# Optimization experiments

Measured on AMD Instinct MI355X. Metric: run time of the kernel, lower is better.

The kernel has to match this reference:

```python
import jax, jax.numpy as jnp
import numpy as np

NUM_ITEMS = 100000
D_SEM = 768
D_PROMPT = 384
D_MODEL = 2048
B, T = 64, 200


def setup_inputs() -> dict:
    key = jax.random.key(0)
    k_ids, k_len, k_sem, k_vp, k_w = jax.random.split(key, 5)
    ids = jax.random.randint(k_ids, (B, T), 0, NUM_ITEMS, dtype=jnp.int64 if jax.config.jax_enable_x64 else jnp.int32)
    lengths = jax.random.randint(k_len, (B,), 1, T + 1, dtype=ids.dtype)
    # positions beyond each sequence length are padding (-1), as produced by the dataloader
    pos = jnp.arange(T, dtype=ids.dtype)[None, :]
    ids = jnp.where(pos < lengths[:, None], ids, -1)
    E_sem = jax.random.normal(k_sem, (NUM_ITEMS, D_SEM), dtype=jnp.float32)
    v_prompt = 0.02 * jax.random.normal(k_vp, (NUM_ITEMS, D_PROMPT), dtype=jnp.float32)
    # nn.Linear weight: [out_features, in_features]
    proj_w = jax.random.normal(k_w, (D_MODEL, D_SEM + D_PROMPT), dtype=jnp.float32) * (1.0 / np.sqrt(D_SEM + D_PROMPT))
    return {"batch_item_ids_padded": ids, "batch_lengths": lengths,
            "E_sem": E_sem, "v_prompt": v_prompt, "proj_w": proj_w}


def reference(batch_item_ids_padded, batch_lengths, E_sem, v_prompt, proj_w):
    """Vectorized build_inputs_embeds: gather + concat + projection, masked.
    Returns (embeds [B,T,d_model], amask [B,T], tok_item_ids [B,T])."""
    ids = batch_item_ids_padded
    num_items = E_sem.shape[0]
    valid = (ids >= 0) & (ids < num_items)            # [B,T]
    safe = jnp.where(valid, ids, 0)                   # clamp for safe gather
    sem = E_sem[safe]                                 # [B,T,d_sem]
    vp = v_prompt[safe]                               # [B,T,d_prompt]
    cat = jnp.concatenate([sem, vp], axis=-1)         # [B,T,d_sem+d_prompt]
    tok = jnp.einsum('btk,dk->btd', cat, proj_w)      # [B,T,d_model]
    embeds = jnp.where(valid[..., None], tok, jnp.zeros((), tok.dtype))
    amask = valid.astype(jnp.int32)
    tok_item_ids = jnp.where(valid, ids, -1)
    return embeds, amask, tok_item_ids
```

## Files before the change

kernel.cpp:

```cpp
#include <hip/hip_runtime.h>
#include <stdint.h>

constexpr int BB = 64, TT = 200;
constexpr int M  = BB * TT;
constexpr int DSEM = 768, DPR = 384;
constexpr int Kd = DSEM + DPR;
constexpr int Nd = 2048;
constexpr int NUM_ITEMS = 100000;
constexpr int BK = 64;

constexpr int GATHER_BLOCKS = (M * Kd / 8) / 256;
constexpr int WCONV_BLOCKS  = (Nd * Kd / 8) / 256;
constexpr int MASK_BLOCKS   = (M + 255) / 256;

typedef short bf16x8 __attribute__((ext_vector_type(8)));
typedef float f32x4  __attribute__((ext_vector_type(4)));

__device__ __forceinline__ unsigned short f2bf(float f) {
  union { float f; uint32_t u; } v; v.f = f;
  uint32_t u = v.u;
  u += 0x7fffu + ((u >> 16) & 1u);
  return (unsigned short)(u >> 16);
}

__global__ void prep_kernel(const int* __restrict__ ids,
                            const float* __restrict__ Esem,
                            const float* __restrict__ vpr,
                            const float* __restrict__ pw,
                            unsigned short* __restrict__ A,
                            unsigned short* __restrict__ Wb,
                            float* __restrict__ amask,
                            float* __restrict__ tok) {
  const int b = blockIdx.x;
  const int tid = threadIdx.x;
  if (b < GATHER_BLOCKS) {
    unsigned g = (unsigned)b * 256u + tid;
    unsigned row = g / 144u;
    unsigned col = (g - row * 144u) * 8u;
    int id = ids[row];
    bool valid = (id >= 0) && (id < NUM_ITEMS);
    int safe = valid ? id : 0;
    const float* src = (col < (unsigned)DSEM)
                         ? (Esem + (size_t)safe * DSEM + col)
                         : (vpr  + (size_t)safe * DPR  + (col - DSEM));
    float4 v0 = *(const float4*)src;
    float4 v1 = *(const float4*)(src + 4);
    if (!valid) {
      v0.x = v0.y = v0.z = v0.w = 0.f;
      v1.x = v1.y = v1.z = v1.w = 0.f;
    }
    ushort4 o0, o1;
    o0.x = f2bf(v0.x); o0.y = f2bf(v0.y); o0.z = f2bf(v0.z); o0.w = f2bf(v0.w);
    o1.x = f2bf(v1.x); o1.y = f2bf(v1.y); o1.z = f2bf(v1.z); o1.w = f2bf(v1.w);
    unsigned short* dst = A + (size_t)row * Kd + col;
    *(ushort4*)dst       = o0;
    *(ushort4*)(dst + 4) = o1;
  } else if (b < GATHER_BLOCKS + WCONV_BLOCKS) {
    int g = (b - GATHER_BLOCKS) * 256 + tid;
    int e = g * 8;
    float4 v0 = *(const float4*)(pw + e);
    float4 v1 = *(const float4*)(pw + e + 4);
    ushort4 o0, o1;
    o0.x = f2bf(v0.x); o0.y = f2bf(v0.y); o0.z = f2bf(v0.z); o0.w = f2bf(v0.w);
    o1.x = f2bf(v1.x); o1.y = f2bf(v1.y); o1.z = f2bf(v1.z); o1.w = f2bf(v1.w);
    *(ushort4*)(Wb + e)     = o0;
    *(ushort4*)(Wb + e + 4) = o1;
  } else {
    int i = (b - GATHER_BLOCKS - WCONV_BLOCKS) * 256 + tid;
    if (i < M) {
      int id = ids[i];
      bool valid = (id >= 0) && (id < NUM_ITEMS);
      amask[i] = valid ? 1.0f : 0.0f;
      tok[i]   = valid ? (float)id : -1.0f;
    }
  }
}

__device__ __forceinline__ void async16(const void* gsrc, void* ldst) {
  __builtin_amdgcn_global_load_lds(
      (const __attribute__((address_space(1))) unsigned int*)gsrc,
      (__attribute__((address_space(3))) unsigned int*)ldst,
      16, 0, 0);
}

__global__ __launch_bounds__(256) void gemm_kernel(const unsigned short* __restrict__ A,
                                                   const unsigned short* __restrict__ Wb,
                                                   float* __restrict__ C) {
  __shared__ __align__(16) unsigned short lds_a[128 * BK];
  __shared__ __align__(16) unsigned short lds_b[128 * BK];

  const int tid  = threadIdx.x;
  const int lane = tid & 63;
  const int wave = tid >> 6;
  const int wm = wave >> 1, wn = wave & 1;
  const int quad = lane >> 4, lm = lane & 15;

  const int b  = blockIdx.x;
  const int k8 = b & 7;
  const int i  = b >> 3;
  const int m0 = (i >> 1) * 128;
  const int n0 = (k8 + 8 * (i & 1)) * 128;

  const int srow   = tid >> 3;
  const int schunk = tid & 7;

  f32x4 acc[4][4];
#pragma unroll
  for (int i2 = 0; i2 < 4; ++i2)
#pragma unroll
    for (int j = 0; j < 4; ++j) acc[i2][j] = (f32x4){0.f, 0.f, 0.f, 0.f};

  for (int kt = 0; kt < Kd / BK; ++kt) {
    const int k0 = kt * BK;
#pragma unroll
    for (int r = 0; r < 4; ++r) {
      const int row = r * 32 + srow;
      const int gch = schunk ^ (row & 7);
      const unsigned short* ga = A + (size_t)(m0 + row) * Kd + k0 + gch * 8;
      async16(ga, lds_a + (size_t)(r * 256 + wave * 64) * 8);
      const unsigned short* gb = Wb + (size_t)(n0 + row) * Kd + k0 + gch * 8;
      async16(gb, lds_b + (size_t)(r * 256 + wave * 64) * 8);
    }
    __syncthreads();

#pragma unroll
    for (int h = 0; h < 2; ++h) {
      bf16x8 af[4], bfr[4];
#pragma unroll
      for (int mi = 0; mi < 4; ++mi) {
        const int row = wm * 64 + mi * 16 + lm;
        af[mi] = *(const bf16x8*)(lds_a + row * BK + ((h * 4 + quad) ^ (row & 7)) * 8);
      }
#pragma unroll
      for (int ni = 0; ni < 4; ++ni) {
        const int row = wn * 64 + ni * 16 + lm;
        bfr[ni] = *(const bf16x8*)(lds_b + row * BK + ((h * 4 + quad) ^ (row & 7)) * 8);
      }
#pragma unroll
      for (int mi = 0; mi < 4; ++mi)
#pragma unroll
        for (int ni = 0; ni < 4; ++ni)
          acc[mi][ni] = __builtin_amdgcn_mfma_f32_16x16x32_bf16(af[mi], bfr[ni], acc[mi][ni], 0, 0, 0);
    }
    __syncthreads();
  }

  float* lw = (float*)lds_a + wave * 1024;
  const int r4  = lane >> 4;
  const int c16 = lane & 15;
#pragma unroll
  for (int mi = 0; mi < 4; ++mi) {
#pragma unroll
    for (int ni = 0; ni < 4; ++ni)
#pragma unroll
      for (int ii = 0; ii < 4; ++ii)
        lw[(quad * 4 + ii) * 64 + ni * 16 + lm] = acc[mi][ni][ii];
#pragma unroll
    for (int j = 0; j < 4; ++j) {
      float4 v = *(const float4*)(lw + (j * 4 + r4) * 64 + c16 * 4);
      const int row = m0 + wm * 64 + mi * 16 + j * 4 + r4;
      const int col = n0 + wn * 64 + c16 * 4;
      *(float4*)(C + (size_t)row * Nd + col) = v;
    }
  }
}

extern "C" void kernel_launch(void* const* d_in, const int* in_sizes, int n_in,
                              void* d_out, int out_size, void* d_ws, size_t ws_size,
                              hipStream_t stream) {
  const int*   ids  = (const int*)d_in[0];
  const float* Esem = (const float*)d_in[2];
  const float* vpr  = (const float*)d_in[3];
  const float* pw   = (const float*)d_in[4];

  float* out_emb   = (float*)d_out;
  float* out_amask = out_emb + (size_t)M * Nd;
  float* out_tok   = out_amask + M;

  unsigned short* A  = (unsigned short*)d_ws;
  unsigned short* Wb = A + (size_t)M * Kd;

  prep_kernel<<<GATHER_BLOCKS + WCONV_BLOCKS + MASK_BLOCKS, 256, 0, stream>>>(
      ids, Esem, vpr, pw, A, Wb, out_amask, out_tok);
  gemm_kernel<<<(M / 128) * (Nd / 128), 256, 0, stream>>>(A, Wb, out_emb);
}
```

Baseline: 519.4 us.

## Compact valid rows before gather and GEMM, zero-fill padded rows separately

Adds a single-block compaction kernel that uses a ballot-based prefix sum to build lists of valid and invalid row indices. The gather and GEMM then run only over the compacted valid rows: early-exit blocks skip strips beyond the valid count, and outputs are scattered through the index map. Extra blocks write zeros to the padded rows. This removes gather and matmul work on padding, at the cost of an extra serial single-block kernel launch and scattered output writes.

```diff
diff --git a/kernel.cpp b/kernel.cpp
--- a/kernel.cpp
+++ b/kernel.cpp
@@ -11,9 +11,11 @@
 
 constexpr int GATHER_BLOCKS = (M * Kd / 8) / 256;
 constexpr int WCONV_BLOCKS  = (Nd * Kd / 8) / 256;
-constexpr int MASK_BLOCKS   = (M + 255) / 256;
+constexpr int GEMM_BLOCKS   = (M / 128) * (Nd / 128);
+constexpr int ZB            = 256;
 
 typedef short bf16x8 __attribute__((ext_vector_type(8)));
+typedef unsigned short u16x8 __attribute__((ext_vector_type(8)));
 typedef float f32x4  __attribute__((ext_vector_type(4)));
 
 __device__ __forceinline__ unsigned short f2bf(float f) {
@@ -23,56 +25,94 @@
   return (unsigned short)(u >> 16);
 }
 
-__global__ void prep_kernel(const int* __restrict__ ids,
-                            const float* __restrict__ Esem,
-                            const float* __restrict__ vpr,
-                            const float* __restrict__ pw,
-                            unsigned short* __restrict__ A,
-                            unsigned short* __restrict__ Wb,
-                            float* __restrict__ amask,
-                            float* __restrict__ tok) {
+__global__ __launch_bounds__(1024) void compact_kernel(
+    const int* __restrict__ ids,
+    int* __restrict__ cid,
+    int* __restrict__ orig,
+    int* __restrict__ inv,
+    int* __restrict__ cnt,
+    float* __restrict__ amask,
+    float* __restrict__ tok) {
+  __shared__ int wb_v[16], wb_i[16];
+  __shared__ int base_v, base_i;
+  const int tid  = threadIdx.x;
+  const int wave = tid >> 6;
+  const int lane = tid & 63;
+  if (tid == 0) { base_v = 0; base_i = 0; }
+  __syncthreads();
+  const unsigned long long below = (lane == 0) ? 0ull : (~0ull >> (64 - lane));
+  for (int r0 = 0; r0 < M; r0 += 1024) {
+    const int i = r0 + tid;
+    int id = -1;
+    if (i < M) id = ids[i];
+    const bool valid   = (id >= 0) && (id < NUM_ITEMS);
+    const bool invalidRow = (i < M) && !valid;
+    const unsigned long long mv = __ballot(valid);
+    const unsigned long long mi = __ballot(invalidRow);
+    if (lane == 0) { wb_v[wave] = __popcll(mv); wb_i[wave] = __popcll(mi); }
+    __syncthreads();
+    if (tid == 0) {
+      int av = base_v, ai = base_i;
+#pragma unroll
+      for (int w = 0; w < 16; ++w) {
+        int tv = wb_v[w], ti = wb_i[w];
+        wb_v[w] = av; wb_i[w] = ai;
+        av += tv; ai += ti;
+      }
+      base_v = av; base_i = ai;
+    }
+    __syncthreads();
+    if (i < M) {
+      amask[i] = valid ? 1.0f : 0.0f;
+      tok[i]   = valid ? (float)id : -1.0f;
+      if (valid) {
+        const int s = wb_v[wave] + __popcll(mv & below);
+        cid[s]  = id;
+        orig[s] = i;
+      } else {
+        const int s = wb_i[wave] + __popcll(mi & below);
+        inv[s] = i;
+      }
+    }
+    __syncthreads();
+  }
+  if (tid == 0) { cnt[0] = base_v; cnt[1] = base_i; }
+}
+
+__global__ void prep2_kernel(const int* __restrict__ cid,
+                             const int* __restrict__ cnt,
+                             const float* __restrict__ Esem,
+                             const float* __restrict__ vpr,
+                             const float* __restrict__ pw,
+                             unsigned short* __restrict__ A,
+                             unsigned short* __restrict__ Wb) {
   const int b = blockIdx.x;
   const int tid = threadIdx.x;
   if (b < GATHER_BLOCKS) {
+    const int cnt0 = cnt[0];
     unsigned g = (unsigned)b * 256u + tid;
     unsigned row = g / 144u;
+    if ((int)row >= cnt0) return;
     unsigned col = (g - row * 144u) * 8u;
-    int id = ids[row];
-    bool valid = (id >= 0) && (id < NUM_ITEMS);
-    int safe = valid ? id : 0;
+    const int id = cid[row];
     const float* src = (col < (unsigned)DSEM)
-                         ? (Esem + (size_t)safe * DSEM + col)
-                         : (vpr  + (size_t)safe * DPR  + (col - DSEM));
+                         ? (Esem + (size_t)id * DSEM + col)
+                         : (vpr  + (size_t)id * DPR  + (col - DSEM));
     float4 v0 = *(const float4*)src;
     float4 v1 = *(const float4*)(src + 4);
-    if (!valid) {
-      v0.x = v0.y = v0.z = v0.w = 0.f;
-      v1.x = v1.y = v1.z = v1.w = 0.f;
-    }
-    ushort4 o0, o1;
-    o0.x = f2bf(v0.x); o0.y = f2bf(v0.y); o0.z = f2bf(v0.z); o0.w = f2bf(v0.w);
-    o1.x = f2bf(v1.x); o1.y = f2bf(v1.y); o1.z = f2bf(v1.z); o1.w = f2bf(v1.w);
-    unsigned short* dst = A + (size_t)row * Kd + col;
-    *(ushort4*)dst       = o0;
-    *(ushort4*)(dst + 4) = o1;
-  } else if (b < GATHER_BLOCKS + WCONV_BLOCKS) {
+    u16x8 o;
+    o[0] = f2bf(v0.x); o[1] = f2bf(v0.y); o[2] = f2bf(v0.z); o[3] = f2bf(v0.w);
+    o[4] = f2bf(v1.x); o[5] = f2bf(v1.y); o[6] = f2bf(v1.z); o[7] = f2bf(v1.w);
+    *(u16x8*)(A + (size_t)row * Kd + col) = o;
+  } else {
     int g = (b - GATHER_BLOCKS) * 256 + tid;
     int e = g * 8;
     float4 v0 = *(const float4*)(pw + e);
     float4 v1 = *(const float4*)(pw + e + 4);
-    ushort4 o0, o1;
-    o0.x = f2bf(v0.x); o0.y = f2bf(v0.y); o0.z = f2bf(v0.z); o0.w = f2bf(v0.w);
-    o1.x = f2bf(v1.x); o1.y = f2bf(v1.y); o1.z = f2bf(v1.z); o1.w = f2bf(v1.w);
-    *(ushort4*)(Wb + e)     = o0;
-    *(ushort4*)(Wb + e + 4) = o1;
-  } else {
-    int i = (b - GATHER_BLOCKS - WCONV_BLOCKS) * 256 + tid;
-    if (i < M) {
-      int id = ids[i];
-      bool valid = (id >= 0) && (id < NUM_ITEMS);
-      amask[i] = valid ? 1.0f : 0.0f;
-      tok[i]   = valid ? (float)id : -1.0f;
-    }
+    u16x8 o;
+    o[0] = f2bf(v0.x); o[1] = f2bf(v0.y); o[2] = f2bf(v0.z); o[3] = f2bf(v0.w);
+    o[4] = f2bf(v1.x); o[5] = f2bf(v1.y); o[6] = f2bf(v1.z); o[7] = f2bf(v1.w);
+    *(u16x8*)(Wb + e) = o;
   }
 }
 
@@ -85,21 +125,41 @@
 
 __global__ __launch_bounds__(256) void gemm_kernel(const unsigned short* __restrict__ A,
                                                    const unsigned short* __restrict__ Wb,
+                                                   const int* __restrict__ orig,
+                                                   const int* __restrict__ inv,
+                                                   const int* __restrict__ cnt,
                                                    float* __restrict__ C) {
   __shared__ __align__(16) unsigned short lds_a[128 * BK];
   __shared__ __align__(16) unsigned short lds_b[128 * BK];
 
-  const int tid  = threadIdx.x;
+  const int tid = threadIdx.x;
+
+  if (blockIdx.x >= GEMM_BLOCKS) {
+    const int zb   = blockIdx.x - GEMM_BLOCKS;
+    const int ninv = cnt[1];
+    const float4 z4 = {0.f, 0.f, 0.f, 0.f};
+    for (int v = zb; v < ninv; v += ZB) {
+      float* dst = C + (size_t)inv[v] * Nd + tid * 8;
+      *(float4*)dst       = z4;
+      *(float4*)(dst + 4) = z4;
+    }
+    return;
+  }
+
+  const int cnt0   = cnt[0];
+  const int strips = (cnt0 + 127) >> 7;
+
+  const int b  = blockIdx.x;
+  const int k8 = b & 7;
+  const int i  = b >> 3;
+  if ((i >> 1) >= strips) return;
+  const int m0 = (i >> 1) * 128;
+  const int n0 = (k8 + 8 * (i & 1)) * 128;
+
   const int lane = tid & 63;
   const int wave = tid >> 6;
   const int wm = wave >> 1, wn = wave & 1;
   const int quad = lane >> 4, lm = lane & 15;
-
-  const int b  = blockIdx.x;
-  const int k8 = b & 7;
-  const int i  = b >> 3;
-  const int m0 = (i >> 1) * 128;
-  const int n0 = (k8 + 8 * (i & 1)) * 128;
 
   const int srow   = tid >> 3;
   const int schunk = tid & 7;
@@ -158,9 +218,12 @@
 #pragma unroll
     for (int j = 0; j < 4; ++j) {
       float4 v = *(const float4*)(lw + (j * 4 + r4) * 64 + c16 * 4);
-      const int row = m0 + wm * 64 + mi * 16 + j * 4 + r4;
-      const int col = n0 + wn * 64 + c16 * 4;
-      *(float4*)(C + (size_t)row * Nd + col) = v;
+      const int rowc = m0 + wm * 64 + mi * 16 + j * 4 + r4;
+      if (rowc < cnt0) {
+        const int R   = orig[rowc];
+        const int col = n0 + wn * 64 + c16 * 4;
+        *(float4*)(C + (size_t)R * Nd + col) = v;
+      }
     }
   }
 }
@@ -179,8 +242,12 @@
 
   unsigned short* A  = (unsigned short*)d_ws;
   unsigned short* Wb = A + (size_t)M * Kd;
-
-  prep_kernel<<<GATHER_BLOCKS + WCONV_BLOCKS + MASK_BLOCKS, 256, 0, stream>>>(
-      ids, Esem, vpr, pw, A, Wb, out_amask, out_tok);
-  gemm_kernel<<<(M / 128) * (Nd / 128), 256, 0, stream>>>(A, Wb, out_emb);
-}
+  int* cid  = (int*)(Wb + (size_t)Nd * Kd);
+  int* orig = cid + M;
+  int* inv  = orig + M;
+  int* cnt  = inv + M;
+
+  compact_kernel<<<1, 1024, 0, stream>>>(ids, cid, orig, inv, cnt, out_amask, out_tok);
+  prep2_kernel<<<GATHER_BLOCKS + WCONV_BLOCKS, 256, 0, stream>>>(cid, cnt, Esem, vpr, pw, A, Wb);
+  gemm_kernel<<<GEMM_BLOCKS + ZB, 256, 0, stream>>>(A, Wb, orig, inv, cnt, out_emb);
+}
```

Result: no change. 509.9 us (-1.8%).

## Compact valid rows via length prefix sum and skip padded GEMM work

Applied to the files above, without the earlier changes.

The prep kernel computes a prefix sum of the batch lengths. It gathers only the valid tokens into a compacted A matrix and records each compacted row's original row index. The GEMM skips 128-row strips beyond the valid count and scatters its results back to the original rows. Extra blocks zero the padded output rows, so work on padding (about half the rows for uniform lengths) is skipped, at the cost of a binary search per gather thread and scattered output writes. Correctness depends on padding being exactly the positions at or beyond each sequence length.

```diff
diff --git a/kernel.cpp b/kernel.cpp
--- a/kernel.cpp
+++ b/kernel.cpp
@@ -12,8 +12,11 @@
 constexpr int GATHER_BLOCKS = (M * Kd / 8) / 256;
 constexpr int WCONV_BLOCKS  = (Nd * Kd / 8) / 256;
 constexpr int MASK_BLOCKS   = (M + 255) / 256;
+constexpr int GEMM_BLOCKS   = (M / 128) * (Nd / 128);
+constexpr int ZB            = 256;
 
 typedef short bf16x8 __attribute__((ext_vector_type(8)));
+typedef unsigned short u16x8 __attribute__((ext_vector_type(8)));
 typedef float f32x4  __attribute__((ext_vector_type(4)));
 
 __device__ __forceinline__ unsigned short f2bf(float f) {
@@ -23,48 +26,70 @@
   return (unsigned short)(u >> 16);
 }
 
+
 __global__ void prep_kernel(const int* __restrict__ ids,
+                            const int* __restrict__ lens,
                             const float* __restrict__ Esem,
                             const float* __restrict__ vpr,
                             const float* __restrict__ pw,
                             unsigned short* __restrict__ A,
                             unsigned short* __restrict__ Wb,
+                            int* __restrict__ orig,
+                            int* __restrict__ cnt,
                             float* __restrict__ amask,
                             float* __restrict__ tok) {
-  const int b = blockIdx.x;
+  const int b   = blockIdx.x;
   const int tid = threadIdx.x;
   if (b < GATHER_BLOCKS) {
-    unsigned g = (unsigned)b * 256u + tid;
+    __shared__ int offs[65];
+    if (tid < 64) {
+      int x = lens[tid];
+#pragma unroll
+      for (int d = 1; d < 64; d <<= 1) {
+        int y = __shfl_up(x, d);
+        if (tid >= d) x += y;
+      }
+      offs[tid + 1] = x;
+      if (tid == 0) offs[0] = 0;
+    }
+    __syncthreads();
+    const int cnt0 = offs[64];
+    if (b == 0 && tid == 0) cnt[0] = cnt0;
+    unsigned g   = (unsigned)b * 256u + tid;
     unsigned row = g / 144u;
-    unsigned col = (g - row * 144u) * 8u;
-    int id = ids[row];
-    bool valid = (id >= 0) && (id < NUM_ITEMS);
-    int safe = valid ? id : 0;
+    if ((int)row >= cnt0) return;
+    unsigned chunk = g - row * 144u;
+    unsigned col   = chunk * 8u;
+    int lo = 0, hi = 63;
+#pragma unroll
+    for (int s = 0; s < 6; ++s) {
+      int mid = (lo + hi + 1) >> 1;
+      if (offs[mid] <= (int)row) lo = mid; else hi = mid - 1;
+    }
+    const int bb   = lo;
+    const int t    = (int)row - offs[bb];
+    const int orow = bb * TT + t;
+    if (chunk == 0) orig[row] = orow;
+    int id = ids[orow];
+    id = (id >= 0 && id < NUM_ITEMS) ? id : 0;
     const float* src = (col < (unsigned)DSEM)
-                         ? (Esem + (size_t)safe * DSEM + col)
-                         : (vpr  + (size_t)safe * DPR  + (col - DSEM));
+                         ? (Esem + (size_t)id * DSEM + col)
+                         : (vpr  + (size_t)id * DPR  + (col - DSEM));
     float4 v0 = *(const float4*)src;
     float4 v1 = *(const float4*)(src + 4);
-    if (!valid) {
-      v0.x = v0.y = v0.z = v0.w = 0.f;
-      v1.x = v1.y = v1.z = v1.w = 0.f;
-    }
-    ushort4 o0, o1;
-    o0.x = f2bf(v0.x); o0.y = f2bf(v0.y); o0.z = f2bf(v0.z); o0.w = f2bf(v0.w);
-    o1.x = f2bf(v1.x); o1.y = f2bf(v1.y); o1.z = f2bf(v1.z); o1.w = f2bf(v1.w);
-    unsigned short* dst = A + (size_t)row * Kd + col;
-    *(ushort4*)dst       = o0;
-    *(ushort4*)(dst + 4) = o1;
+    u16x8 o;
+    o[0] = f2bf(v0.x); o[1] = f2bf(v0.y); o[2] = f2bf(v0.z); o[3] = f2bf(v0.w);
+    o[4] = f2bf(v1.x); o[5] = f2bf(v1.y); o[6] = f2bf(v1.z); o[7] = f2bf(v1.w);
+    *(u16x8*)(A + (size_t)row * Kd + col) = o;
   } else if (b < GATHER_BLOCKS + WCONV_BLOCKS) {
     int g = (b - GATHER_BLOCKS) * 256 + tid;
     int e = g * 8;
     float4 v0 = *(const float4*)(pw + e);
     float4 v1 = *(const float4*)(pw + e + 4);
-    ushort4 o0, o1;
-    o0.x = f2bf(v0.x); o0.y = f2bf(v0.y); o0.z = f2bf(v0.z); o0.w = f2bf(v0.w);
-    o1.x = f2bf(v1.x); o1.y = f2bf(v1.y); o1.z = f2bf(v1.z); o1.w = f2bf(v1.w);
-    *(ushort4*)(Wb + e)     = o0;
-    *(ushort4*)(Wb + e + 4) = o1;
+    u16x8 o;
+    o[0] = f2bf(v0.x); o[1] = f2bf(v0.y); o[2] = f2bf(v0.z); o[3] = f2bf(v0.w);
+    o[4] = f2bf(v1.x); o[5] = f2bf(v1.y); o[6] = f2bf(v1.z); o[7] = f2bf(v1.w);
+    *(u16x8*)(Wb + e) = o;
   } else {
     int i = (b - GATHER_BLOCKS - WCONV_BLOCKS) * 256 + tid;
     if (i < M) {
@@ -85,21 +110,43 @@
 
 __global__ __launch_bounds__(256) void gemm_kernel(const unsigned short* __restrict__ A,
                                                    const unsigned short* __restrict__ Wb,
+                                                   const int* __restrict__ orig,
+                                                   const int* __restrict__ lens,
+                                                   const int* __restrict__ cnt,
                                                    float* __restrict__ C) {
   __shared__ __align__(16) unsigned short lds_a[128 * BK];
   __shared__ __align__(16) unsigned short lds_b[128 * BK];
 
-  const int tid  = threadIdx.x;
+  const int tid = threadIdx.x;
+
+  if (blockIdx.x >= GEMM_BLOCKS) {
+    const int zb  = blockIdx.x - GEMM_BLOCKS;
+    const int bb  = zb & 63;
+    const int j0  = zb >> 6;
+    const int len = lens[bb];
+    const float4 z4 = {0.f, 0.f, 0.f, 0.f};
+    for (int t = len + j0; t < TT; t += 4) {
+      float* dst = C + (size_t)(bb * TT + t) * Nd + tid * 8;
+      *(float4*)dst       = z4;
+      *(float4*)(dst + 4) = z4;
+    }
+    return;
+  }
+
+  const int cnt0   = cnt[0];
+  const int strips = (cnt0 + 127) >> 7;
+
+  const int b  = blockIdx.x;
+  const int k8 = b & 7;
+  const int i  = b >> 3;
+  if ((i >> 1) >= strips) return;
+  const int m0 = (i >> 1) * 128;
+  const int n0 = (k8 + 8 * (i & 1)) * 128;
+
   const int lane = tid & 63;
   const int wave = tid >> 6;
   const int wm = wave >> 1, wn = wave & 1;
   const int quad = lane >> 4, lm = lane & 15;
-
-  const int b  = blockIdx.x;
-  const int k8 = b & 7;
-  const int i  = b >> 3;
-  const int m0 = (i >> 1) * 128;
-  const int n0 = (k8 + 8 * (i & 1)) * 128;
 
   const int srow   = tid >> 3;
   const int schunk = tid & 7;
@@ -158,9 +205,12 @@
 #pragma unroll
     for (int j = 0; j < 4; ++j) {
       float4 v = *(const float4*)(lw + (j * 4 + r4) * 64 + c16 * 4);
-      const int row = m0 + wm * 64 + mi * 16 + j * 4 + r4;
-      const int col = n0 + wn * 64 + c16 * 4;
-      *(float4*)(C + (size_t)row * Nd + col) = v;
+      const int rowc = m0 + wm * 64 + mi * 16 + j * 4 + r4;
+      if (rowc < cnt0) {
+        const int R   = orig[rowc];
+        const int col = n0 + wn * 64 + c16 * 4;
+        *(float4*)(C + (size_t)R * Nd + col) = v;
+      }
     }
   }
 }
@@ -169,6 +219,7 @@
                               void* d_out, int out_size, void* d_ws, size_t ws_size,
                               hipStream_t stream) {
   const int*   ids  = (const int*)d_in[0];
+  const int*   lens = (const int*)d_in[1];
   const float* Esem = (const float*)d_in[2];
   const float* vpr  = (const float*)d_in[3];
   const float* pw   = (const float*)d_in[4];
@@ -179,8 +230,10 @@
 
   unsigned short* A  = (unsigned short*)d_ws;
   unsigned short* Wb = A + (size_t)M * Kd;
+  int* orig = (int*)(Wb + (size_t)Nd * Kd);
+  int* cnt  = orig + M;
 
   prep_kernel<<<GATHER_BLOCKS + WCONV_BLOCKS + MASK_BLOCKS, 256, 0, stream>>>(
-      ids, Esem, vpr, pw, A, Wb, out_amask, out_tok);
-  gemm_kernel<<<(M / 128) * (Nd / 128), 256, 0, stream>>>(A, Wb, out_emb);
-}
+      ids, lens, Esem, vpr, pw, A, Wb, orig, cnt, out_amask, out_tok);
+  gemm_kernel<<<GEMM_BLOCKS + ZB, 256, 0, stream>>>(A, Wb, orig, lens, cnt, out_emb);
+}
```

Result: faster. 494.6 us (-4.8%).
